# Kernel tuning notes

Measured on AMD Instinct MI355X. Metric: run time of the kernel, lower is better.

Reference implementation:

```python
import jax, jax.numpy as jnp
import numpy as np

N_NODES = 20000


def gcn_layer(x, W, b, src, dst, n):
    # linear transform first (as in PyG GCNConv)
    h = x @ W  # [N, out]
    # add self-loops
    loop = jnp.arange(n, dtype=src.dtype)
    src_f = jnp.concatenate([src, loop])
    dst_f = jnp.concatenate([dst, loop])
    # symmetric degree normalization: deg computed on destination (col) index
    ones = jnp.ones_like(dst_f, dtype=h.dtype)
    deg = jax.ops.segment_sum(ones, dst_f, num_segments=n)
    dinv = jnp.where(deg > 0, jax.lax.rsqrt(deg), 0.0)
    norm = dinv[src_f] * dinv[dst_f]  # [E+N]
    # gather-normalize-scatter aggregation
    msgs = h[src_f] * norm[:, None]  # [E+N, out]
    out = jax.ops.segment_sum(msgs, dst_f, num_segments=n)
    return out + b


def setup_inputs() -> dict:
    key = jax.random.key(0)
    k = jax.random.split(key, 6)
    x = jax.random.normal(k[0], (N_NODES, 256), dtype=jnp.float32)
    edge_index = jax.random.randint(k[1], (2, 320000), 0, N_NODES, dtype=jnp.int64)
    s1 = 1.0 / np.sqrt(256)
    s2 = 1.0 / np.sqrt(1600)
    W1 = jax.random.uniform(k[2], (256, 1600), jnp.float32, -s1, s1)
    b1 = jnp.zeros((1600,), jnp.float32)
    W2 = jax.random.uniform(k[3], (1600, 400), jnp.float32, -s2, s2)
    b2 = jnp.zeros((400,), jnp.float32)
    return {"x": x, "edge_index": edge_index, "W1": W1, "b1": b1, "W2": W2, "b2": b2}


def reference(x, edge_index, W1, b1, W2, b2):
    src, dst = edge_index[0], edge_index[1]
    n = x.shape[0]
    h = jax.nn.relu(gcn_layer(x, W1, b1, src, dst, n))
    return gcn_layer(h, W2, b2, src, dst, n)
```

## Files before the change

### kernel.cpp

```cpp
#include <hip/hip_runtime.h>
#include <hip/hip_bf16.h>
#include <stdint.h>

typedef _Float16 f16;
typedef _Float16 f16x8 __attribute__((ext_vector_type(8)));
typedef _Float16 f16v4 __attribute__((ext_vector_type(4)));
typedef float f32x4 __attribute__((ext_vector_type(4)));

__device__ __forceinline__ void gload_lds16(const f16* g, f16* l) {
  __builtin_amdgcn_global_load_lds(
      (const __attribute__((address_space(1))) void*)g,
      (__attribute__((address_space(3))) void*)l, 16, 0, 0);
}

__device__ __forceinline__ int edge_at(const void* ep, int isI64, long long idx) {
  if (isI64) return (int)((const long long*)ep)[idx];
  return ((const int*)ep)[idx];
}

__global__ void detect_kernel(const unsigned int* __restrict__ e, int* __restrict__ flag) {
  __shared__ int any;
  if (threadIdx.x == 0) any = 0;
  __syncthreads();
  for (int idx = 1 + 2 * (int)threadIdx.x; idx < 4096; idx += 512) {
    if (e[idx] != 0u) any = 1;
  }
  __syncthreads();
  if (threadIdx.x == 0) flag[0] = any ? 0 : 1;
}

__global__ void deg_kernel(const void* __restrict__ ep, const int* __restrict__ flag,
                           int* __restrict__ indeg, int E) {
  int e = blockIdx.x * blockDim.x + threadIdx.x;
  if (e >= E) return;
  int i64 = flag[0];
  int d = edge_at(ep, i64, (long long)E + e);
  atomicAdd(&indeg[d], 1);
}

__global__ __launch_bounds__(1024) void prefix_kernel(const int* __restrict__ indeg,
                                                      int* __restrict__ rowptr,
                                                      float* __restrict__ dinv, int n) {
  __shared__ int wsum[16];
  int t = threadIdx.x;
  int lane = t & 63;
  int w = t >> 6;
  int carry = 0;
  if (t == 0) rowptr[0] = 0;
  for (int base = 0; base < n; base += 1024) {
    int i = base + t;
    int v = (i < n) ? indeg[i] : 0;
    if (i < n) dinv[i] = rsqrtf((float)(v + 1));
    int sv = v;
#pragma unroll
    for (int off = 1; off < 64; off <<= 1) {
      int u = __shfl_up(sv, off, 64);
      if (lane >= off) sv += u;
    }
    if (lane == 63) wsum[w] = sv;
    __syncthreads();
    if (w == 0 && lane < 16) {
      int ws = wsum[lane];
#pragma unroll
      for (int off = 1; off < 16; off <<= 1) {
        int u = __shfl_up(ws, off, 64);
        if (lane >= off) ws += u;
      }
      wsum[lane] = ws;
    }
    __syncthreads();
    int woff = (w > 0) ? wsum[w - 1] : 0;
    if (i < n) rowptr[i + 1] = carry + woff + sv;
    carry += wsum[15];
    __syncthreads();
  }
}

__global__ void scatter_kernel(const void* __restrict__ ep, const int* __restrict__ flag,
                               const int* __restrict__ rowptr, int* __restrict__ cursor,
                               int* __restrict__ colsrc, int E) {
  int e = blockIdx.x * blockDim.x + threadIdx.x;
  if (e >= E) return;
  int i64 = flag[0];
  int s = edge_at(ep, i64, (long long)e);
  int d = edge_at(ep, i64, (long long)E + e);
  int pos = atomicAdd(&cursor[d], 1);
  colsrc[rowptr[d] + pos] = s;
}

__global__ void xcast_kernel(const float* __restrict__ x, const float* __restrict__ dinv,
                             f16* __restrict__ xs, int n) {
  int c = blockIdx.x * 256 + threadIdx.x;
  if (c >= n * 64) return;
  int row = c >> 6;
  float d = dinv[row];
  float4 v = ((const float4*)x)[c];
  f16v4 r;
  r[0] = (f16)(d * v.x);
  r[1] = (f16)(d * v.y);
  r[2] = (f16)(d * v.z);
  r[3] = (f16)(d * v.w);
  ((f16v4*)xs)[c] = r;
}

__global__ __launch_bounds__(256) void agg1_kernel(const f16* __restrict__ xs,
                                                   const float* __restrict__ dinv,
                                                   const int* __restrict__ rowptr,
                                                   const int* __restrict__ colsrc,
                                                   f16* __restrict__ xa, int n) {
  int wave = threadIdx.x >> 6;
  int lane = threadIdx.x & 63;
  int i = blockIdx.x * 4 + wave;
  if (i >= n) return;
  const f16v4* xp = (const f16v4*)xs;
  float di = dinv[i];
  f16v4 s = xp[(size_t)i * 64 + lane];
  float a0 = (float)s[0], a1 = (float)s[1], a2 = (float)s[2], a3 = (float)s[3];
  float b0 = 0.f, b1 = 0.f, b2 = 0.f, b3 = 0.f;
  int beg = rowptr[i], end = rowptr[i + 1];
  int j = beg;
  for (; j + 3 < end; j += 4) {
    int s0 = colsrc[j], s1 = colsrc[j + 1], s2 = colsrc[j + 2], s3 = colsrc[j + 3];
    f16v4 v0 = xp[(size_t)s0 * 64 + lane];
    f16v4 v1 = xp[(size_t)s1 * 64 + lane];
    f16v4 v2 = xp[(size_t)s2 * 64 + lane];
    f16v4 v3 = xp[(size_t)s3 * 64 + lane];
    a0 += (float)v0[0] + (float)v2[0]; a1 += (float)v0[1] + (float)v2[1];
    a2 += (float)v0[2] + (float)v2[2]; a3 += (float)v0[3] + (float)v2[3];
    b0 += (float)v1[0] + (float)v3[0]; b1 += (float)v1[1] + (float)v3[1];
    b2 += (float)v1[2] + (float)v3[2]; b3 += (float)v1[3] + (float)v3[3];
  }
  for (; j < end; ++j) {
    int s0 = colsrc[j];
    f16v4 v0 = xp[(size_t)s0 * 64 + lane];
    a0 += (float)v0[0]; a1 += (float)v0[1]; a2 += (float)v0[2]; a3 += (float)v0[3];
  }
  f16v4 r;
  r[0] = (f16)(di * (a0 + b0));
  r[1] = (f16)(di * (a1 + b1));
  r[2] = (f16)(di * (a2 + b2));
  r[3] = (f16)(di * (a3 + b3));
  *(f16v4*)&xa[(size_t)i * 256 + lane * 4] = r;
}

__global__ __launch_bounds__(256) void agg2_kernel(const f16* __restrict__ gs,
                                                   const float* __restrict__ dinv,
                                                   const int* __restrict__ rowptr,
                                                   const int* __restrict__ colsrc,
                                                   const float* __restrict__ bias,
                                                   float* __restrict__ out, int n, int F) {
  int wave = threadIdx.x >> 6;
  int lane = threadIdx.x & 63;
  int i = blockIdx.x * 4 + wave;
  if (i >= n) return;
  int base = lane * 8;
  if (base >= F) return;
  float di = dinv[i];
  f16x8 sv = *(const f16x8*)&gs[(size_t)i * F + base];
  float a[8], b[8];
#pragma unroll
  for (int r = 0; r < 8; ++r) { a[r] = (float)sv[r]; b[r] = 0.f; }
  int beg = rowptr[i], end = rowptr[i + 1];
  int j = beg;
  for (; j + 3 < end; j += 4) {
    int s0 = colsrc[j], s1 = colsrc[j + 1], s2 = colsrc[j + 2], s3 = colsrc[j + 3];
    f16x8 v0 = *(const f16x8*)&gs[(size_t)s0 * F + base];
    f16x8 v1 = *(const f16x8*)&gs[(size_t)s1 * F + base];
    f16x8 v2 = *(const f16x8*)&gs[(size_t)s2 * F + base];
    f16x8 v3 = *(const f16x8*)&gs[(size_t)s3 * F + base];
#pragma unroll
    for (int r = 0; r < 8; ++r) {
      a[r] += (float)v0[r] + (float)v2[r];
      b[r] += (float)v1[r] + (float)v3[r];
    }
  }
  for (; j < end; ++j) {
    int s0 = colsrc[j];
    f16x8 v0 = *(const f16x8*)&gs[(size_t)s0 * F + base];
#pragma unroll
    for (int r = 0; r < 8; ++r) a[r] += (float)v0[r];
  }
  float4 o0, o1;
  float4 bv0 = *(const float4*)&bias[base];
  float4 bv1 = *(const float4*)&bias[base + 4];
  o0.x = di * (a[0] + b[0]) + bv0.x; o0.y = di * (a[1] + b[1]) + bv0.y;
  o0.z = di * (a[2] + b[2]) + bv0.z; o0.w = di * (a[3] + b[3]) + bv0.w;
  o1.x = di * (a[4] + b[4]) + bv1.x; o1.y = di * (a[5] + b[5]) + bv1.y;
  o1.z = di * (a[6] + b[6]) + bv1.z; o1.w = di * (a[7] + b[7]) + bv1.w;
  *(float4*)&out[(size_t)i * F + base] = o0;
  *(float4*)&out[(size_t)i * F + base + 4] = o1;
}

__global__ void castT_kernel(const float* __restrict__ W1, f16* __restrict__ W1t, int K1, int N1,
                             const float* __restrict__ W2, f16* __restrict__ W2t, int K2, int N2) {
  int idx = blockIdx.x * 256 + threadIdx.x;
  int t1 = K1 * N1;
  if (idx < t1) {
    int k = idx / N1;
    int nn = idx - k * N1;
    W1t[(size_t)nn * K1 + k] = (f16)W1[idx];
  } else {
    idx -= t1;
    if (idx < K2 * N2) {
      int k = idx / N2;
      int nn = idx - k * N2;
      W2t[(size_t)nn * K2 + k] = (f16)W2[idx];
    }
  }
}

__global__ __launch_bounds__(256) void gemm1_f16(
    const f16* __restrict__ A, const f16* __restrict__ B,
    const float* __restrict__ bias, f16* __restrict__ C,
    int M, int N, int K) {
  __shared__ __align__(16) f16 smem[2 * 128 * 64];
  f16* sA = smem;
  f16* sB = smem + 128 * 64;
  const int m0 = blockIdx.y * 128;
  const int n0 = blockIdx.x * 128;
  const int lane = threadIdx.x & 63;
  const int wave = threadIdx.x >> 6;
  const int wm = (wave & 1) * 64;
  const int wn = (wave >> 1) * 64;
  const int lrow = lane & 15;
  const int quad = lane >> 4;

  f32x4 acc[4][4];
#pragma unroll
  for (int i = 0; i < 4; ++i)
#pragma unroll
    for (int j = 0; j < 4; ++j) acc[i][j] = (f32x4)(0.f);

  for (int k0 = 0; k0 < K; k0 += 64) {
#pragma unroll
    for (int i = 0; i < 4; ++i) {
      int ch = (i * 4 + wave) * 64 + lane;
      int r = ch >> 3;
      int cg = (ch & 7) ^ (r & 7);
      int gr = min(m0 + r, M - 1);
      gload_lds16(&A[(size_t)gr * K + k0 + cg * 8], &sA[(size_t)(i * 4 + wave) * 512]);
      int gn = min(n0 + r, N - 1);
      gload_lds16(&B[(size_t)gn * K + k0 + cg * 8], &sB[(size_t)(i * 4 + wave) * 512]);
    }
    __syncthreads();
#pragma unroll
    for (int kk = 0; kk < 2; ++kk) {
      f16x8 af[4], bf[4];
      int cg = quad + kk * 4;
#pragma unroll
      for (int i = 0; i < 4; ++i) {
        int ra = wm + i * 16 + lrow;
        af[i] = *(const f16x8*)&sA[ra * 64 + ((cg ^ (ra & 7)) * 8)];
        int rb = wn + i * 16 + lrow;
        bf[i] = *(const f16x8*)&sB[rb * 64 + ((cg ^ (rb & 7)) * 8)];
      }
#pragma unroll
      for (int i = 0; i < 4; ++i)
#pragma unroll
        for (int j = 0; j < 4; ++j)
          acc[i][j] = __builtin_amdgcn_mfma_f32_16x16x32_f16(af[i], bf[j], acc[i][j], 0, 0, 0);
    }
    __syncthreads();
  }

  const int crow = quad * 4;
  const int ccol = lane & 15;
#pragma unroll
  for (int j = 0; j < 4; ++j) {
    int col = wn + j * 16 + ccol;
    int gcol = n0 + col;
    float bv = (gcol < N) ? bias[gcol] : 0.f;
#pragma unroll
    for (int i = 0; i < 4; ++i) {
#pragma unroll
      for (int r = 0; r < 4; ++r) {
        int row = wm + i * 16 + crow + r;
        smem[row * 128 + col] = (f16)fmaxf(acc[i][j][r] + bv, 0.f);
      }
    }
  }
  __syncthreads();
#pragma unroll
  for (int i = 0; i < 8; ++i) {
    int ch = i * 256 + (int)threadIdx.x;
    int r = ch >> 4;
    int cc = ch & 15;
    int grow = m0 + r;
    int gcol = n0 + cc * 8;
    if (grow < M && gcol < N)
      *(uint4*)&C[(size_t)grow * N + gcol] = *(const uint4*)&smem[r * 128 + cc * 8];
  }
}

__global__ __launch_bounds__(256) void gemm2_f16(
    const f16* __restrict__ A, const f16* __restrict__ B,
    const float* __restrict__ dinv, f16* __restrict__ C,
    int M, int N, int K) {
  __shared__ __align__(16) f16 smem[128 * 64 + 80 * 64];
  f16* sA = smem;
  f16* sB = smem + 128 * 64;

  const int mtc = (M + 127) >> 7;
  const int ntc = (N + 79) / 80;
  const int fullm = mtc & ~7;
  const int full = fullm * ntc;
  int idf = blockIdx.x;
  int mt, nt;
  if (idf < full) {
    int gsz = 8 * ntc;
    int grp = idf / gsz;
    int r = idf - grp * gsz;
    mt = grp * 8 + (r & 7);
    nt = r >> 3;
  } else {
    int r = idf - full;
    int rem = mtc - fullm;
    mt = fullm + r % rem;
    nt = r / rem;
  }
  const int m0 = mt * 128;
  const int n0 = nt * 80;
  const int lane = threadIdx.x & 63;
  const int wave = threadIdx.x >> 6;
  const int wm = wave * 32;
  const int lrow = lane & 15;
  const int quad = lane >> 4;

  f32x4 acc[2][5];
#pragma unroll
  for (int i = 0; i < 2; ++i)
#pragma unroll
    for (int j = 0; j < 5; ++j) acc[i][j] = (f32x4)(0.f);

  for (int k0 = 0; k0 < K; k0 += 64) {
#pragma unroll
    for (int i = 0; i < 4; ++i) {
      int ch = (i * 4 + wave) * 64 + lane;
      int r = ch >> 3;
      int cg = (ch & 7) ^ (r & 7);
      int gr = min(m0 + r, M - 1);
      gload_lds16(&A[(size_t)gr * K + k0 + cg * 8], &sA[(size_t)(i * 4 + wave) * 512]);
    }
#pragma unroll
    for (int i = 0; i < 3; ++i) {
      if (i * 4 + wave < 10) {
        int ch = (i * 4 + wave) * 64 + lane;
        int r = ch >> 3;
        int cg = (ch & 7) ^ (r & 7);
        gload_lds16(&B[(size_t)(n0 + r) * K + k0 + cg * 8], &sB[(size_t)(i * 4 + wave) * 512]);
      }
    }
    __syncthreads();
#pragma unroll
    for (int kk = 0; kk < 2; ++kk) {
      f16x8 af[2], bf[5];
      int cg = quad + kk * 4;
#pragma unroll
      for (int i = 0; i < 2; ++i) {
        int ra = wm + i * 16 + lrow;
        af[i] = *(const f16x8*)&sA[ra * 64 + ((cg ^ (ra & 7)) * 8)];
      }
#pragma unroll
      for (int j = 0; j < 5; ++j) {
        int rb = j * 16 + lrow;
        bf[j] = *(const f16x8*)&sB[rb * 64 + ((cg ^ (rb & 7)) * 8)];
      }
#pragma unroll
      for (int i = 0; i < 2; ++i)
#pragma unroll
        for (int j = 0; j < 5; ++j)
          acc[i][j] = __builtin_amdgcn_mfma_f32_16x16x32_f16(af[i], bf[j], acc[i][j], 0, 0, 0);
    }
    __syncthreads();
  }

  const int crow = quad * 4;
  const int ccol = lane & 15;
  float dsc[2][4];
#pragma unroll
  for (int i = 0; i < 2; ++i)
#pragma unroll
    for (int r = 0; r < 4; ++r) {
      int grow = m0 + wm + i * 16 + crow + r;
      dsc[i][r] = dinv[min(grow, M - 1)];
    }
#pragma unroll
  for (int j = 0; j < 5; ++j) {
    int col = j * 16 + ccol;
#pragma unroll
    for (int i = 0; i < 2; ++i) {
#pragma unroll
      for (int r = 0; r < 4; ++r) {
        int row = wm + i * 16 + crow + r;
        smem[row * 80 + col] = (f16)(acc[i][j][r] * dsc[i][r]);
      }
    }
  }
  __syncthreads();
#pragma unroll
  for (int i = 0; i < 5; ++i) {
    int ch = i * 256 + (int)threadIdx.x;
    int r = ch / 10;
    int rem = ch - 10 * r;
    int grow = m0 + r;
    if (grow < M)
      *(uint4*)&C[(size_t)grow * N + n0 + rem * 8] = *(const uint4*)&smem[r * 80 + rem * 8];
  }
}

extern "C" void kernel_launch(void* const* d_in, const int* in_sizes, int n_in,
                              void* d_out, int out_size, void* d_ws, size_t ws_size,
                              hipStream_t stream) {
  const float* x = (const float*)d_in[0];
  const void* edges = d_in[1];
  const float* W1 = (const float*)d_in[2];
  const float* b1 = (const float*)d_in[3];
  const float* W2 = (const float*)d_in[4];
  const float* b2 = (const float*)d_in[5];
  float* out = (float*)d_out;

  const int N1 = in_sizes[3];
  const int N2 = in_sizes[5];
  const int K1 = in_sizes[2] / N1;
  const int K2 = in_sizes[4] / N2;
  const int n = in_sizes[0] / K1;
  const int E = in_sizes[1] / 2;

  char* ws = (char*)d_ws;
  size_t o = 0;
  auto take = [&](size_t bytes) {
    char* p = ws + o;
    o += (bytes + 255) & ~(size_t)255;
    return p;
  };
  int* indeg = (int*)take((size_t)n * 4);
  int* cursor = (int*)take((size_t)n * 4);
  int* flag = (int*)take(4);
  size_t zero_bytes = o;
  int* rowptr = (int*)take((size_t)(n + 1) * 4);
  int* colsrc = (int*)take((size_t)E * 4);
  float* dinv = (float*)take((size_t)n * 4);
  f16* xs = (f16*)take((size_t)n * K1 * 2);
  f16* xa = (f16*)take((size_t)n * K1 * 2);
  f16* w1t = (f16*)take((size_t)K1 * N1 * 2);
  f16* w2t = (f16*)take((size_t)K2 * N2 * 2);
  f16* h = (f16*)take((size_t)n * N1 * 2);
  f16* g = (f16*)take((size_t)n * N2 * 2);

  hipMemsetAsync(d_ws, 0, zero_bytes, stream);

  detect_kernel<<<1, 256, 0, stream>>>((const unsigned int*)edges, flag);
  deg_kernel<<<(E + 255) / 256, 256, 0, stream>>>(edges, flag, indeg, E);
  prefix_kernel<<<1, 1024, 0, stream>>>(indeg, rowptr, dinv, n);
  scatter_kernel<<<(E + 255) / 256, 256, 0, stream>>>(edges, flag, rowptr, cursor, colsrc, E);

  castT_kernel<<<(K1 * N1 + K2 * N2 + 255) / 256, 256, 0, stream>>>(W1, w1t, K1, N1, W2, w2t,
                                                                    K2, N2);
  xcast_kernel<<<(n * 64 + 255) / 256, 256, 0, stream>>>(x, dinv, xs, n);

  agg1_kernel<<<(n + 3) / 4, 256, 0, stream>>>(xs, dinv, rowptr, colsrc, xa, n);
  {
    dim3 grid((N1 + 127) / 128, (n + 127) / 128);
    gemm1_f16<<<grid, 256, 0, stream>>>(xa, w1t, b1, h, n, N1, K1);
  }
  {
    int mtc = (n + 127) / 128;
    int ntc = (N2 + 79) / 80;
    gemm2_f16<<<mtc * ntc, 256, 0, stream>>>(h, w2t, dinv, g, n, N2, K2);
  }
  agg2_kernel<<<(n + 3) / 4, 256, 0, stream>>>(g, dinv, rowptr, colsrc, b2, out, n, N2);
}
```

Baseline: 291.9 us.

## Parallelize degree prefix scan across blocks and shrink GEMM2 M-tile to 64

Replaces the single-block serial prefix scan over 20 nodes' degrees with a three-kernel reduce/scan/apply scan spread across ~20 blocks. Halves the GEMM2 M tile from 128 to 64 rows, so each wave computes a 16x80 tile and the grid doubles to fill more CUs. The smaller GEMM tile lowers per-block A reuse and MFMA density, and the scan adds two extra kernel launches. The B loads are also clamped to N-1.

```diff
diff --git a/kernel.cpp b/kernel.cpp
--- a/kernel.cpp
+++ b/kernel.cpp
@@ -38,42 +38,69 @@
   atomicAdd(&indeg[d], 1);
 }
 
-__global__ __launch_bounds__(1024) void prefix_kernel(const int* __restrict__ indeg,
-                                                      int* __restrict__ rowptr,
-                                                      float* __restrict__ dinv, int n) {
+__global__ __launch_bounds__(1024) void scan1_kernel(const int* __restrict__ indeg,
+                                                     float* __restrict__ dinv,
+                                                     int* __restrict__ bsum, int n) {
+  __shared__ int ws[16];
+  int t = threadIdx.x;
+  int i = blockIdx.x * 1024 + t;
+  int v = (i < n) ? indeg[i] : 0;
+  if (i < n) dinv[i] = rsqrtf((float)(v + 1));
+  int s = v;
+#pragma unroll
+  for (int off = 32; off > 0; off >>= 1) s += __shfl_down(s, off, 64);
+  if ((t & 63) == 0) ws[t >> 6] = s;
+  __syncthreads();
+  if (t < 16) {
+    int x = ws[t];
+#pragma unroll
+    for (int off = 8; off > 0; off >>= 1) x += __shfl_down(x, off, 64);
+    if (t == 0) bsum[blockIdx.x] = x;
+  }
+}
+
+__global__ void scan2_kernel(const int* __restrict__ bsum, int* __restrict__ boff, int nb) {
+  int lane = threadIdx.x;
+  int v = (lane < nb) ? bsum[lane] : 0;
+  int sv = v;
+#pragma unroll
+  for (int off = 1; off < 64; off <<= 1) {
+    int u = __shfl_up(sv, off, 64);
+    if (lane >= off) sv += u;
+  }
+  if (lane < nb) boff[lane] = sv - v;
+}
+
+__global__ __launch_bounds__(1024) void scan3_kernel(const int* __restrict__ indeg,
+                                                     const int* __restrict__ boff,
+                                                     int* __restrict__ rowptr, int n) {
   __shared__ int wsum[16];
   int t = threadIdx.x;
   int lane = t & 63;
   int w = t >> 6;
-  int carry = 0;
-  if (t == 0) rowptr[0] = 0;
-  for (int base = 0; base < n; base += 1024) {
-    int i = base + t;
-    int v = (i < n) ? indeg[i] : 0;
-    if (i < n) dinv[i] = rsqrtf((float)(v + 1));
-    int sv = v;
-#pragma unroll
-    for (int off = 1; off < 64; off <<= 1) {
-      int u = __shfl_up(sv, off, 64);
-      if (lane >= off) sv += u;
-    }
-    if (lane == 63) wsum[w] = sv;
-    __syncthreads();
-    if (w == 0 && lane < 16) {
-      int ws = wsum[lane];
-#pragma unroll
-      for (int off = 1; off < 16; off <<= 1) {
-        int u = __shfl_up(ws, off, 64);
-        if (lane >= off) ws += u;
-      }
-      wsum[lane] = ws;
-    }
-    __syncthreads();
-    int woff = (w > 0) ? wsum[w - 1] : 0;
-    if (i < n) rowptr[i + 1] = carry + woff + sv;
-    carry += wsum[15];
-    __syncthreads();
-  }
+  int i = blockIdx.x * 1024 + t;
+  int v = (i < n) ? indeg[i] : 0;
+  int sv = v;
+#pragma unroll
+  for (int off = 1; off < 64; off <<= 1) {
+    int u = __shfl_up(sv, off, 64);
+    if (lane >= off) sv += u;
+  }
+  if (lane == 63) wsum[w] = sv;
+  __syncthreads();
+  if (w == 0 && lane < 16) {
+    int x = wsum[lane];
+#pragma unroll
+    for (int off = 1; off < 16; off <<= 1) {
+      int u = __shfl_up(x, off, 64);
+      if (lane >= off) x += u;
+    }
+    wsum[lane] = x;
+  }
+  __syncthreads();
+  int woff = (w > 0) ? wsum[w - 1] : 0;
+  if (i < n) rowptr[i + 1] = boff[blockIdx.x] + woff + sv;
+  if (i == 0) rowptr[0] = 0;
 }
 
 __global__ void scatter_kernel(const void* __restrict__ ep, const int* __restrict__ flag,
@@ -296,11 +323,11 @@
     const f16* __restrict__ A, const f16* __restrict__ B,
     const float* __restrict__ dinv, f16* __restrict__ C,
     int M, int N, int K) {
-  __shared__ __align__(16) f16 smem[128 * 64 + 80 * 64];
+  __shared__ __align__(16) f16 smem[64 * 64 + 80 * 64];
   f16* sA = smem;
-  f16* sB = smem + 128 * 64;
-
-  const int mtc = (M + 127) >> 7;
+  f16* sB = smem + 64 * 64;
+
+  const int mtc = (M + 63) >> 6;
   const int ntc = (N + 79) / 80;
   const int fullm = mtc & ~7;
   const int full = fullm * ntc;
@@ -318,23 +345,20 @@
     mt = fullm + r % rem;
     nt = r / rem;
   }
-  const int m0 = mt * 128;
+  const int m0 = mt * 64;
   const int n0 = nt * 80;
   const int lane = threadIdx.x & 63;
   const int wave = threadIdx.x >> 6;
-  const int wm = wave * 32;
   const int lrow = lane & 15;
   const int quad = lane >> 4;
 
-  f32x4 acc[2][5];
-#pragma unroll
-  for (int i = 0; i < 2; ++i)
-#pragma unroll
-    for (int j = 0; j < 5; ++j) acc[i][j] = (f32x4)(0.f);
+  f32x4 acc[5];
+#pragma unroll
+  for (int j = 0; j < 5; ++j) acc[j] = (f32x4)(0.f);
 
   for (int k0 = 0; k0 < K; k0 += 64) {
 #pragma unroll
-    for (int i = 0; i < 4; ++i) {
+    for (int i = 0; i < 2; ++i) {
       int ch = (i * 4 + wave) * 64 + lane;
       int r = ch >> 3;
       int cg = (ch & 7) ^ (r & 7);
@@ -347,64 +371,57 @@
         int ch = (i * 4 + wave) * 64 + lane;
         int r = ch >> 3;
         int cg = (ch & 7) ^ (r & 7);
-        gload_lds16(&B[(size_t)(n0 + r) * K + k0 + cg * 8], &sB[(size_t)(i * 4 + wave) * 512]);
+        int gn = min(n0 + r, N - 1);
+        gload_lds16(&B[(size_t)gn * K + k0 + cg * 8], &sB[(size_t)(i * 4 + wave) * 512]);
       }
     }
     __syncthreads();
 #pragma unroll
     for (int kk = 0; kk < 2; ++kk) {
-      f16x8 af[2], bf[5];
       int cg = quad + kk * 4;
-#pragma unroll
-      for (int i = 0; i < 2; ++i) {
-        int ra = wm + i * 16 + lrow;
-        af[i] = *(const f16x8*)&sA[ra * 64 + ((cg ^ (ra & 7)) * 8)];
-      }
+      int ra = wave * 16 + lrow;
+      f16x8 af = *(const f16x8*)&sA[ra * 64 + ((cg ^ (ra & 7)) * 8)];
+      f16x8 bf[5];
 #pragma unroll
       for (int j = 0; j < 5; ++j) {
         int rb = j * 16 + lrow;
         bf[j] = *(const f16x8*)&sB[rb * 64 + ((cg ^ (rb & 7)) * 8)];
       }
 #pragma unroll
-      for (int i = 0; i < 2; ++i)
-#pragma unroll
-        for (int j = 0; j < 5; ++j)
-          acc[i][j] = __builtin_amdgcn_mfma_f32_16x16x32_f16(af[i], bf[j], acc[i][j], 0, 0, 0);
+      for (int j = 0; j < 5; ++j)
+        acc[j] = __builtin_amdgcn_mfma_f32_16x16x32_f16(af, bf[j], acc[j], 0, 0, 0);
     }
     __syncthreads();
   }
 
   const int crow = quad * 4;
   const int ccol = lane & 15;
-  float dsc[2][4];
-#pragma unroll
-  for (int i = 0; i < 2; ++i)
-#pragma unroll
-    for (int r = 0; r < 4; ++r) {
-      int grow = m0 + wm + i * 16 + crow + r;
-      dsc[i][r] = dinv[min(grow, M - 1)];
-    }
+  float dsc[4];
+#pragma unroll
+  for (int r = 0; r < 4; ++r) {
+    int grow = m0 + wave * 16 + crow + r;
+    dsc[r] = dinv[min(grow, M - 1)];
+  }
 #pragma unroll
   for (int j = 0; j < 5; ++j) {
     int col = j * 16 + ccol;
 #pragma unroll
-    for (int i = 0; i < 2; ++i) {
-#pragma unroll
-      for (int r = 0; r < 4; ++r) {
-        int row = wm + i * 16 + crow + r;
-        smem[row * 80 + col] = (f16)(acc[i][j][r] * dsc[i][r]);
-      }
-    }
-  }
-  __syncthreads();
-#pragma unroll
-  for (int i = 0; i < 5; ++i) {
+    for (int r = 0; r < 4; ++r) {
+      int row = wave * 16 + crow + r;
+      smem[row * 80 + col] = (f16)(acc[j][r] * dsc[r]);
+    }
+  }
+  __syncthreads();
+#pragma unroll
+  for (int i = 0; i < 3; ++i) {
     int ch = i * 256 + (int)threadIdx.x;
-    int r = ch / 10;
-    int rem = ch - 10 * r;
-    int grow = m0 + r;
-    if (grow < M)
-      *(uint4*)&C[(size_t)grow * N + n0 + rem * 8] = *(const uint4*)&smem[r * 80 + rem * 8];
+    if (ch < 640) {
+      int r = ch / 10;
+      int rem = ch - 10 * r;
+      int grow = m0 + r;
+      if (grow < M)
+        *(uint4*)&C[(size_t)grow * N + n0 + rem * 8] = *(const uint4*)&smem[r * 80 + rem * 8];
+    }
   }
 }
 
@@ -440,6 +457,8 @@
   int* rowptr = (int*)take((size_t)(n + 1) * 4);
   int* colsrc = (int*)take((size_t)E * 4);
   float* dinv = (float*)take((size_t)n * 4);
+  int* bsum = (int*)take(64 * 4);
+  int* boff = (int*)take(64 * 4);
   f16* xs = (f16*)take((size_t)n * K1 * 2);
   f16* xa = (f16*)take((size_t)n * K1 * 2);
   f16* w1t = (f16*)take((size_t)K1 * N1 * 2);
@@ -449,9 +468,13 @@
 
   hipMemsetAsync(d_ws, 0, zero_bytes, stream);
 
+  const int nb = (n + 1023) / 1024;
+
   detect_kernel<<<1, 256, 0, stream>>>((const unsigned int*)edges, flag);
   deg_kernel<<<(E + 255) / 256, 256, 0, stream>>>(edges, flag, indeg, E);
-  prefix_kernel<<<1, 1024, 0, stream>>>(indeg, rowptr, dinv, n);
+  scan1_kernel<<<nb, 1024, 0, stream>>>(indeg, dinv, bsum, n);
+  scan2_kernel<<<1, 64, 0, stream>>>(bsum, boff, nb);
+  scan3_kernel<<<nb, 1024, 0, stream>>>(indeg, boff, rowptr, n);
   scatter_kernel<<<(E + 255) / 256, 256, 0, stream>>>(edges, flag, rowptr, cursor, colsrc, E);
 
   castT_kernel<<<(K1 * N1 + K2 * N2 + 255) / 256, 256, 0, stream>>>(W1, w1t, K1, N1, W2, w2t,
@@ -464,7 +487,7 @@
     gemm1_f16<<<grid, 256, 0, stream>>>(xa, w1t, b1, h, n, N1, K1);
   }
   {
-    int mtc = (n + 127) / 128;
+    int mtc = (n + 63) / 64;
     int ntc = (N2 + 79) / 80;
     gemm2_f16<<<mtc * ntc, 256, 0, stream>>>(h, w2t, dinv, g, n, N2, K2);
   }
```

New measurement: 279.6 us. 1.04x faster.
